# Performance work log

Measured on AMD Instinct MI355X. Metric: run time of the kernel, lower is better.

Reference implementation:

```python
import jax, jax.numpy as jnp
import numpy as np

DIM, D_STATE, D_CONV, EXPAND = 768, 16, 4, 2
D_INNER = EXPAND * DIM
DT_RANK = (DIM + 15) // 16  # 48
B_SZ, L_SZ = 4, 4096


def setup_inputs() -> dict:
    key = jax.random.key(0)
    ks = jax.random.split(key, 20)
    s = 0.02
    d = {}
    d['x'] = jax.random.normal(ks[0], (B_SZ, L_SZ, DIM), jnp.float32)
    d['in_proj_w'] = jax.random.normal(ks[1], (2 * D_INNER, DIM), jnp.float32) * s
    d['out_proj_w'] = jax.random.normal(ks[2], (DIM, D_INNER), jnp.float32) * s
    # forward-direction params
    d['conv1d_w'] = jax.random.normal(ks[3], (D_INNER, 1, D_CONV), jnp.float32) * s
    d['conv1d_bias'] = jax.random.normal(ks[4], (D_INNER,), jnp.float32) * s
    d['x_proj_w'] = jax.random.normal(ks[5], (DT_RANK + 2 * D_STATE, D_INNER), jnp.float32) * s
    d['dt_proj_w'] = jax.random.normal(ks[6], (D_INNER, DT_RANK), jnp.float32) * s
    d['dt_proj_bias'] = jax.random.normal(ks[7], (D_INNER,), jnp.float32) * 0.1 - 4.0
    d['A_log'] = jnp.log(jax.random.uniform(ks[8], (D_INNER, D_STATE), jnp.float32, 1.0, 16.0))
    d['D'] = jax.random.normal(ks[9], (D_INNER,), jnp.float32) * 0.1 + 1.0
    # backward-direction params (bimamba v2)
    d['conv1d_w_b'] = jax.random.normal(ks[10], (D_INNER, 1, D_CONV), jnp.float32) * s
    d['conv1d_bias_b'] = jax.random.normal(ks[11], (D_INNER,), jnp.float32) * s
    d['x_proj_w_b'] = jax.random.normal(ks[12], (DT_RANK + 2 * D_STATE, D_INNER), jnp.float32) * s
    d['dt_proj_w_b'] = jax.random.normal(ks[13], (D_INNER, DT_RANK), jnp.float32) * s
    d['dt_proj_bias_b'] = jax.random.normal(ks[14], (D_INNER,), jnp.float32) * 0.1 - 4.0
    d['A_log_b'] = jnp.log(jax.random.uniform(ks[15], (D_INNER, D_STATE), jnp.float32, 1.0, 16.0))
    d['D_b'] = jax.random.normal(ks[16], (D_INNER,), jnp.float32) * 0.1 + 1.0
    return d


def _causal_depthwise_conv(x, w, b):
    # x: (B, D, L), w: (D, 1, K) depthwise, causal left padding
    k = w.shape[-1]
    xp = jnp.pad(x, ((0, 0), (0, 0), (k - 1, 0)))
    y = jax.lax.conv_general_dilated(
        xp, w, window_strides=(1,), padding='VALID',
        dimension_numbers=('NCH', 'OIH', 'NCH'), feature_group_count=x.shape[1])
    return y + b[None, :, None]


def _selective_scan(u, dt, A, B, C, D):
    # u, dt: (b, d, l); A: (d, n); B, C: (b, n, l); D: (d,)
    b, d, l = u.shape
    n = A.shape[1]

    def step(h, inp):
        u_t, dt_t, B_t, C_t = inp  # (b,d) (b,d) (b,n) (b,n)
        dA = jnp.exp(dt_t[..., None] * A)  # (b,d,n)
        h = h * dA + dt_t[..., None] * B_t[:, None, :] * u_t[..., None]
        y = jnp.einsum('bdn,bn->bd', h, C_t)
        return h, y

    h0 = jnp.zeros((b, d, n), u.dtype)
    xs = (jnp.moveaxis(u, 2, 0), jnp.moveaxis(dt, 2, 0),
          jnp.moveaxis(B, 2, 0), jnp.moveaxis(C, 2, 0))
    _, ys = jax.lax.scan(step, h0, xs)  # ys: (l, b, d)
    y = jnp.moveaxis(ys, 0, 2)  # (b, d, l)
    return y + u * D[None, :, None]


def _one_direction(xz, conv_w, conv_b, x_proj_w, dt_w, dt_b, A_log, D):
    d_inner = xz.shape[1] // 2
    xin, z = xz[:, :d_inner], xz[:, d_inner:]  # (b,d,l) each
    xc = jax.nn.silu(_causal_depthwise_conv(xin, conv_w, conv_b))
    x_dbl = jnp.einsum('bdl,cd->bcl', xc, x_proj_w)  # (b, dt_rank+2n, l)
    dt_r = x_dbl[:, :DT_RANK]
    Bm = x_dbl[:, DT_RANK:DT_RANK + D_STATE]
    Cm = x_dbl[:, DT_RANK + D_STATE:]
    dt = jax.nn.softplus(jnp.einsum('brl,dr->bdl', dt_r, dt_w) + dt_b[None, :, None])
    A = -jnp.exp(A_log)
    y = _selective_scan(xc, dt, A, Bm, Cm, D)
    return y * jax.nn.silu(z)


def reference(x, in_proj_w, out_proj_w,
              conv1d_w, conv1d_bias, x_proj_w, dt_proj_w, dt_proj_bias, A_log, D,
              conv1d_w_b, conv1d_bias_b, x_proj_w_b, dt_proj_w_b, dt_proj_bias_b, A_log_b, D_b):
    # x: (B, L, dim)
    xz = jnp.einsum('bld,ed->bel', x, in_proj_w)  # (b, 2*d_inner, l)
    out_f = _one_direction(xz, conv1d_w, conv1d_bias, x_proj_w,
                           dt_proj_w, dt_proj_bias, A_log, D)
    out_r = _one_direction(xz[:, :, ::-1], conv1d_w_b, conv1d_bias_b, x_proj_w_b,
                           dt_proj_w_b, dt_proj_bias_b, A_log_b, D_b)
    out = out_f + out_r[:, :, ::-1]  # (b, d_inner, l)
    return jnp.einsum('bdl,od->blo', out, out_proj_w)  # (b, l, dim)
```

## Files before the change

### kernel.cpp

```cpp
#include <hip/hip_runtime.h>

#define L_SZ   4096
#define B_SZ   4
#define NCOLS  16384
#define DIM    768
#define DINNER 1536
#define E2     3072
#define DTRANK 48
#define DSTATE 16
#define NCHUNK 64
#define CLEN   64


typedef unsigned short ushortT;
typedef __attribute__((ext_vector_type(8))) short short8;
typedef __attribute__((ext_vector_type(4))) float floatx4;

__device__ __forceinline__ unsigned short f2bf(float f) {
  union { float f; unsigned u; } v; v.f = f;
  unsigned r = v.u + 0x7FFF + ((v.u >> 16) & 1);
  return (unsigned short)(r >> 16);
}
__device__ __forceinline__ float bf2f(unsigned short h) {
  union { unsigned u; float f; } v; v.u = ((unsigned)h) << 16;
  return v.f;
}

__global__ __launch_bounds__(256) void cvt_bf16_kernel(const float* __restrict__ in,
                                                       ushortT* __restrict__ out, int n4) {
  int i = blockIdx.x * 256 + threadIdx.x;
  if (i >= n4) return;
  float4 v = ((const float4*)in)[i];
  ushort4 o;
  o.x = f2bf(v.x); o.y = f2bf(v.y); o.z = f2bf(v.z); o.w = f2bf(v.w);
  ((ushort4*)out)[i] = o;
}

__global__ __launch_bounds__(256) void zero_kernel(float4* __restrict__ p) {
  p[blockIdx.x * 256 + threadIdx.x] = make_float4(0.f, 0.f, 0.f, 0.f);
}

__global__ __launch_bounds__(256) void gemm_nt(const ushortT* __restrict__ A,
                                               const ushortT* __restrict__ Bm,
                                               float* __restrict__ Cf, ushortT* __restrict__ Cb,
                                               int M, int N, int K, int out_bf16, int G)
{
  __shared__ ushortT As[128 * 64];
  __shared__ ushortT Bs[128 * 64];
  int tid = threadIdx.x;
  int wave = tid >> 6, lane = tid & 63;
  int gid = blockIdx.y * gridDim.x + blockIdx.x;
  int per_sg = G * gridDim.y;
  int sg = gid / per_sg, r = gid % per_sg;
  int bm = r / G;
  int bn = sg * G + (r % G);
  const ushortT* Abase = A + (size_t)bm * 128 * K;
  const ushortT* Bbase = Bm + (size_t)bn * 128 * K;
  int lm = lane & 15, lq = lane >> 4;
  int wm = (wave >> 1) * 64, wn = (wave & 1) * 64;
  int rloc = lane >> 3;
  int c_st = (lane & 7) * 8;
  floatx4 acc[4][4] = {};

  for (int k0 = 0; k0 < K; k0 += 64) {
    __syncthreads();
    #pragma unroll
    for (int j = 0; j < 4; j++) {
      int t = wave * 4 + j;
      const ushortT* ga = Abase + (size_t)(t * 8 + rloc) * K + k0 + c_st;
      const ushortT* gb = Bbase + (size_t)(t * 8 + rloc) * K + k0 + c_st;
      __builtin_amdgcn_global_load_lds((const __attribute__((address_space(1))) void*)ga,
                                       (__attribute__((address_space(3))) void*)(As + t * 512),
                                       16, 0, 0);
      __builtin_amdgcn_global_load_lds((const __attribute__((address_space(1))) void*)gb,
                                       (__attribute__((address_space(3))) void*)(Bs + t * 512),
                                       16, 0, 0);
    }
    __syncthreads();
    #pragma unroll
    for (int ks = 0; ks < 2; ks++) {
      short8 af[4], bfv[4];
      #pragma unroll
      for (int i = 0; i < 4; i++)
        af[i] = *(const short8*)(As + (wm + i * 16 + lm) * 64 + ks * 32 + lq * 8);
      #pragma unroll
      for (int j2 = 0; j2 < 4; j2++)
        bfv[j2] = *(const short8*)(Bs + (wn + j2 * 16 + lm) * 64 + ks * 32 + lq * 8);
      #pragma unroll
      for (int i = 0; i < 4; i++)
        #pragma unroll
        for (int j2 = 0; j2 < 4; j2++)
          acc[i][j2] = __builtin_amdgcn_mfma_f32_16x16x32_bf16(af[i], bfv[j2], acc[i][j2], 0, 0, 0);
    }
  }
  #pragma unroll
  for (int i = 0; i < 4; i++) {
    #pragma unroll
    for (int j2 = 0; j2 < 4; j2++) {
      int mg = bm * 128 + wm + i * 16 + lq * 4;
      int ng = bn * 128 + wn + j2 * 16 + lm;
      #pragma unroll
      for (int q = 0; q < 4; q++) {
        size_t off = (size_t)(mg + q) * N + ng;
        if (out_bf16) Cb[off] = f2bf(acc[i][j2][q]);
        else          Cf[off] = acc[i][j2][q];
      }
    }
  }
}

__global__ __launch_bounds__(256) void conv_silu_kernel(const ushortT* __restrict__ xz,
                                                        const float* __restrict__ w,
                                                        const float* __restrict__ bias,
                                                        ushortT* __restrict__ xc, int reverse)
{
  int idx = blockIdx.x * 256 + threadIdx.x;
  int p4 = idx & 1023;
  int rb = idx >> 10;
  int b = rb & 3, d = rb >> 2;
  int wq = p4 >> 6, c = p4 & 63;
  int l0 = c * 64 + wq * 4;
  const ushortT* xin = xz + (size_t)d * NCOLS + b * L_SZ;
  float w0 = w[d * 4], w1 = w[d * 4 + 1], w2 = w[d * 4 + 2], w3 = w[d * 4 + 3];
  float bv = bias[d];
  float xv[8];
  float r0, r1, r2, r3;
  if (!reverse) {
    if (l0 >= 4) {
      ushort4 a = *(const ushort4*)(xin + l0 - 4);
      ushort4 cc = *(const ushort4*)(xin + l0);
      xv[0]=bf2f(a.x); xv[1]=bf2f(a.y); xv[2]=bf2f(a.z); xv[3]=bf2f(a.w);
      xv[4]=bf2f(cc.x); xv[5]=bf2f(cc.y); xv[6]=bf2f(cc.z); xv[7]=bf2f(cc.w);
    } else {
      #pragma unroll
      for (int i = 0; i < 8; i++) { int p = l0 - 4 + i; xv[i] = (p >= 0) ? bf2f(xin[p]) : 0.f; }
    }
    r0 = bv + w0*xv[1] + w1*xv[2] + w2*xv[3] + w3*xv[4];
    r1 = bv + w0*xv[2] + w1*xv[3] + w2*xv[4] + w3*xv[5];
    r2 = bv + w0*xv[3] + w1*xv[4] + w2*xv[5] + w3*xv[6];
    r3 = bv + w0*xv[4] + w1*xv[5] + w2*xv[6] + w3*xv[7];
  } else {
    int base = 4092 - l0;
    if (l0 >= 4) {
      ushort4 a = *(const ushort4*)(xin + base);
      ushort4 cc = *(const ushort4*)(xin + base + 4);
      xv[0]=bf2f(a.x); xv[1]=bf2f(a.y); xv[2]=bf2f(a.z); xv[3]=bf2f(a.w);
      xv[4]=bf2f(cc.x); xv[5]=bf2f(cc.y); xv[6]=bf2f(cc.z); xv[7]=bf2f(cc.w);
    } else {
      #pragma unroll
      for (int i = 0; i < 8; i++) { int p = base + i; xv[i] = (p <= 4095) ? bf2f(xin[p]) : 0.f; }
    }
    r0 = bv + w0*xv[6] + w1*xv[5] + w2*xv[4] + w3*xv[3];
    r1 = bv + w0*xv[5] + w1*xv[4] + w2*xv[3] + w3*xv[2];
    r2 = bv + w0*xv[4] + w1*xv[3] + w2*xv[2] + w3*xv[1];
    r3 = bv + w0*xv[3] + w1*xv[2] + w2*xv[1] + w3*xv[0];
  }
  ushort4 o;
  o.x = f2bf(r0 / (1.f + __expf(-r0)));
  o.y = f2bf(r1 / (1.f + __expf(-r1)));
  o.z = f2bf(r2 / (1.f + __expf(-r2)));
  o.w = f2bf(r3 / (1.f + __expf(-r3)));
  *(ushort4*)(xc + (size_t)d * NCOLS + b * L_SZ + p4 * 4) = o;
}

__global__ __launch_bounds__(256) void xdbl_kernel(const ushortT* __restrict__ xc,
                                                   const float* __restrict__ W,
                                                   float* __restrict__ dtr,
                                                   float* __restrict__ Bt,
                                                   float* __restrict__ Ct)
{
  __shared__ float xcs[32 * 68];
  __shared__ float Ws[80 * 32];
  int tid = threadIdx.x;
  int n0 = blockIdx.x * 64;
  int kbase = blockIdx.y * 512;
  int tm = tid >> 4, tn = tid & 15;
  float acc[5][4] = {};
  for (int k0 = kbase; k0 < kbase + 512; k0 += 32) {
    __syncthreads();
    {
      int kk = tid >> 3, c8 = (tid & 7) * 8;
      const ushortT* src = xc + (size_t)(k0 + kk) * NCOLS + n0 + c8;
      ushort4 a = *(const ushort4*)src;
      ushort4 b = *(const ushort4*)(src + 4);
      float* dst = xcs + kk * 68 + c8;
      dst[0]=bf2f(a.x); dst[1]=bf2f(a.y); dst[2]=bf2f(a.z); dst[3]=bf2f(a.w);
      dst[4]=bf2f(b.x); dst[5]=bf2f(b.y); dst[6]=bf2f(b.z); dst[7]=bf2f(b.w);
    }
    for (int i = tid; i < 80 * 32; i += 256) {
      int m = i >> 5, kk = i & 31;
      Ws[i] = W[(size_t)m * DINNER + k0 + kk];
    }
    __syncthreads();
    #pragma unroll 8
    for (int kk = 0; kk < 32; kk++) {
      const float* xr = xcs + kk * 68 + tn * 4;
      float x0 = xr[0], x1 = xr[1], x2 = xr[2], x3 = xr[3];
      #pragma unroll
      for (int im = 0; im < 5; im++) {
        float wv = Ws[(tm * 5 + im) * 32 + kk];
        acc[im][0] += wv * x0; acc[im][1] += wv * x1;
        acc[im][2] += wv * x2; acc[im][3] += wv * x3;
      }
    }
  }
  #pragma unroll
  for (int im = 0; im < 5; im++) {
    int m = tm * 5 + im;
    #pragma unroll
    for (int j = 0; j < 4; j++) {
      int n = n0 + tn * 4 + j;
      float v = acc[im][j];
      if (m < 48)      atomicAdd(&dtr[(size_t)m * NCOLS + n], v);
      else if (m < 64) atomicAdd(&Bt[(size_t)n * 16 + (m - 48)], v);
      else             atomicAdd(&Ct[(size_t)n * 16 + (m - 64)], v);
    }
  }
}

__global__ __launch_bounds__(256) void dt_kernel(const float* __restrict__ dtr,
                                                 const float* __restrict__ W,
                                                 const float* __restrict__ bias,
                                                 ushortT* __restrict__ dtb)
{
  __shared__ float sD[48 * 68];
  __shared__ float sW[48 * 68];
  int tid = threadIdx.x;
  int n0 = blockIdx.x * 64, d0 = blockIdx.y * 64;
  for (int i = tid; i < 48 * 64; i += 256) {
    int r = i >> 6, c = i & 63;
    sD[r * 68 + c] = dtr[(size_t)r * NCOLS + n0 + c];
  }
  for (int i = tid; i < 64 * 48; i += 256) {
    int dd = i / 48, k = i - dd * 48;
    sW[k * 68 + dd] = W[(size_t)d0 * 48 + i];
  }
  __syncthreads();
  int tn = tid & 15, tm = tid >> 4;
  float acc[4][4];
  #pragma unroll
  for (int i = 0; i < 4; i++) {
    float bv = bias[d0 + tm * 4 + i];
    #pragma unroll
    for (int j = 0; j < 4; j++) acc[i][j] = bv;
  }
  #pragma unroll 6
  for (int k = 0; k < 48; k++) {
    float4 wv = *(const float4*)(sW + k * 68 + tm * 4);
    float4 xv = *(const float4*)(sD + k * 68 + tn * 4);
    float wa[4] = { wv.x, wv.y, wv.z, wv.w };
    float xa[4] = { xv.x, xv.y, xv.z, xv.w };
    #pragma unroll
    for (int i = 0; i < 4; i++)
      #pragma unroll
      for (int j = 0; j < 4; j++)
        acc[i][j] += wa[i] * xa[j];
  }
  #pragma unroll
  for (int i = 0; i < 4; i++) {
    int d = d0 + tm * 4 + i;
    ushort4 o;
    float a0 = acc[i][0], a1 = acc[i][1], a2 = acc[i][2], a3 = acc[i][3];
    o.x = f2bf((a0 > 20.f) ? a0 : log1pf(__expf(a0)));
    o.y = f2bf((a1 > 20.f) ? a1 : log1pf(__expf(a1)));
    o.z = f2bf((a2 > 20.f) ? a2 : log1pf(__expf(a2)));
    o.w = f2bf((a3 > 20.f) ? a3 : log1pf(__expf(a3)));
    *(ushort4*)(dtb + (size_t)d * NCOLS + n0 + tn * 4) = o;
  }
}

__global__ __launch_bounds__(256) void scan_kernel4(ushortT* __restrict__ u,
                                                    const ushortT* __restrict__ dt,
                                                    const float* __restrict__ Bt,
                                                    const float* __restrict__ Ct,
                                                    const float* __restrict__ A_log,
                                                    const float* __restrict__ Dp,
                                                    ushortT* __restrict__ y, int reverse)
{
  __shared__ float Hs[32 * 65];
  __shared__ float Ss[2 * 64];
  int tid = threadIdx.x;
  int hf = tid & 1;
  int c  = (tid >> 1) & 63;
  int dl = tid >> 7;
  int b = blockIdx.y;
  int d = blockIdx.x * 2 + dl;
  int ns0 = hf * 8;

  float Av2[8];
  #pragma unroll
  for (int n = 0; n < 8; n++)
    Av2[n] = -__expf(A_log[d * 16 + ns0 + n]) * 1.442695040888963f;
  float Dv = Dp[d];

  ushortT* ur = u + (size_t)d * NCOLS + b * L_SZ + c * 4;
  const ushortT* tr = dt + (size_t)d * NCOLS + b * L_SZ + c * 4;
  const float*   Bp = Bt + (size_t)b * L_SZ * 16 + ns0;
  const float*   Cp = Ct + (size_t)b * L_SZ * 16 + ns0;

  float h[8];
  float S = 0.f;
  #pragma unroll
  for (int n = 0; n < 8; n++) h[n] = 0.f;

  for (int w = 0; w < 16; w++) {
    ushort4 u4 = *(const ushort4*)(ur + w * 256);
    ushort4 t4 = *(const ushort4*)(tr + w * 256);
    float uv[4] = { bf2f(u4.x), bf2f(u4.y), bf2f(u4.z), bf2f(u4.w) };
    float tv[4] = { bf2f(t4.x), bf2f(t4.y), bf2f(t4.z), bf2f(t4.w) };
    float yo[4];
    #pragma unroll
    for (int q = 0; q < 4; q++) {
      float dtu = tv[q] * uv[q];
      int pl = w * 256 + c * 4 + q;
      const float4* bp4 = (const float4*)(Bp + pl * 16);
      const float4* cp4 = (const float4*)(Cp + pl * 16);
      float4 b0 = bp4[0], b1 = bp4[1];
      float4 c0 = cp4[0], c1 = cp4[1];
      float Bf[8] = { b0.x,b0.y,b0.z,b0.w, b1.x,b1.y,b1.z,b1.w };
      float Cv[8] = { c0.x,c0.y,c0.z,c0.w, c1.x,c1.y,c1.z,c1.w };
      float acc = 0.f;
      #pragma unroll
      for (int n = 0; n < 8; n++) {
        float e = exp2f(tv[q] * Av2[n]);
        h[n] = h[n] * e + Bf[n] * dtu;
        acc += h[n] * Cv[n];
      }
      acc += __shfl_xor(acc, 1);
      yo[q] = acc + Dv * uv[q];
      S += tv[q];
    }
    if (hf == 0) {
      ushort4 o;
      o.x = f2bf(yo[0]); o.y = f2bf(yo[1]); o.z = f2bf(yo[2]); o.w = f2bf(yo[3]);
      *(ushort4*)(ur + w * 256) = o;
    }
  }
  #pragma unroll
  for (int n = 0; n < 8; n++)
    Hs[(dl * 16 + ns0 + n) * 65 + c] = h[n];
  if (hf == 0) Ss[dl * 64 + c] = S;
  __syncthreads();

  if (tid < 32) {
    int dl2 = tid >> 4, n2 = tid & 15;
    float Ac = -__expf(A_log[(blockIdx.x * 2 + dl2) * 16 + n2]) * 1.442695040888963f;
    float hsv = 0.f;
    int row = tid;
    for (int cc = 0; cc < NCHUNK; cc++) {
      int idx = row * 65 + cc;
      float tmp = Hs[idx];
      Hs[idx] = hsv;
      hsv = exp2f(Ac * Ss[dl2 * 64 + cc]) * hsv + tmp;
    }
  }
  __syncthreads();
  float hsr[8];
  #pragma unroll
  for (int n = 0; n < 8; n++) hsr[n] = Hs[(dl * 16 + ns0 + n) * 65 + c];

  ushortT* yrow = y + (size_t)d * NCOLS + b * L_SZ;
  float T = 0.f;
  for (int w = 0; w < 16; w++) {
    ushort4 t4  = *(const ushort4*)(tr + w * 256);
    ushort4 y14 = *(const ushort4*)(ur + w * 256);
    float tv[4]  = { bf2f(t4.x), bf2f(t4.y), bf2f(t4.z), bf2f(t4.w) };
    float y1v[4] = { bf2f(y14.x), bf2f(y14.y), bf2f(y14.z), bf2f(y14.w) };
    float yo[4];
    #pragma unroll
    for (int q = 0; q < 4; q++) {
      T += tv[q];
      int pl = w * 256 + c * 4 + q;
      const float4* cp4 = (const float4*)(Cp + pl * 16);
      float4 c0 = cp4[0], c1 = cp4[1];
      float Cv[8] = { c0.x,c0.y,c0.z,c0.w, c1.x,c1.y,c1.z,c1.w };
      float corr = 0.f;
      #pragma unroll
      for (int n = 0; n < 8; n++)
        corr += (exp2f(Av2[n] * T) * hsr[n]) * Cv[n];
      corr += __shfl_xor(corr, 1);
      yo[q] = y1v[q] + corr;
    }
    if (hf == 0) {
      if (!reverse) {
        ushort4 o;
        o.x = f2bf(yo[0]); o.y = f2bf(yo[1]); o.z = f2bf(yo[2]); o.w = f2bf(yo[3]);
        *(ushort4*)(yrow + w * 256 + c * 4) = o;
      } else {
        ushort4* dst = (ushort4*)(yrow + (15 - w) * 256 + (63 - c) * 4);
        ushort4 old = *dst;
        ushort4 o;
        o.x = f2bf(bf2f(old.x) + yo[3]);
        o.y = f2bf(bf2f(old.y) + yo[2]);
        o.z = f2bf(bf2f(old.z) + yo[1]);
        o.w = f2bf(bf2f(old.w) + yo[0]);
        *dst = o;
      }
    }
  }
}

__global__ __launch_bounds__(256) void inner_kernel(const ushortT* __restrict__ y,
                                                    const ushortT* __restrict__ xz,
                                                    ushortT* __restrict__ innerb)
{
  __shared__ float tile[64 * 65];
  int n0 = blockIdx.x * 64, d0 = blockIdx.y * 64;
  int tid = threadIdx.x;
  int c = tid & 63, rq = tid >> 6;
  int bseg = n0 & ~4095;
  int cch = (n0 & 4095) >> 6;
  int poff = bseg + cch * 4 + (c >> 2) * 256 + (c & 3);
  #pragma unroll
  for (int r = 0; r < 16; r++) {
    int dd = rq + r * 4;
    float yv = bf2f(y[(size_t)(d0 + dd) * NCOLS + poff]);
    float zv = bf2f(xz[(size_t)(DINNER + d0 + dd) * NCOLS + n0 + c]);
    float sv = zv / (1.f + __expf(-zv));
    tile[dd * 65 + c] = yv * sv;
  }
  __syncthreads();
  #pragma unroll
  for (int r = 0; r < 16; r++) {
    int nn = rq + r * 4;
    innerb[(size_t)(n0 + nn) * DINNER + d0 + c] = f2bf(tile[c * 65 + nn]);
  }
}

extern "C" void kernel_launch(void* const* d_in, const int* in_sizes, int n_in,
                              void* d_out, int out_size, void* d_ws, size_t ws_size,
                              hipStream_t stream)
{
  const float* x          = (const float*)d_in[0];
  const float* in_proj_w  = (const float*)d_in[1];
  const float* out_proj_w = (const float*)d_in[2];
  const float* conv_w     = (const float*)d_in[3];
  const float* conv_b     = (const float*)d_in[4];
  const float* xproj_w    = (const float*)d_in[5];
  const float* dt_w       = (const float*)d_in[6];
  const float* dt_b       = (const float*)d_in[7];
  const float* A_log      = (const float*)d_in[8];
  const float* Dp         = (const float*)d_in[9];
  const float* conv_w_b   = (const float*)d_in[10];
  const float* conv_b_b   = (const float*)d_in[11];
  const float* xproj_w_b  = (const float*)d_in[12];
  const float* dt_w_b     = (const float*)d_in[13];
  const float* dt_b_b     = (const float*)d_in[14];
  const float* A_log_b    = (const float*)d_in[15];
  const float* D_b        = (const float*)d_in[16];

  char* ws = (char*)d_ws;
  ushortT* XZ   = (ushortT*)(ws + 0);
  ushortT* XC   = (ushortT*)(ws + 100663296);
  ushortT* YB   = (ushortT*)(ws + 150994944);
  float*   DTR  = (float*)  (ws + 201326592);
  float*   BT   = (float*)  (ws + 204472320);
  float*   CT   = (float*)  (ws + 205520896);
  ushortT* WOB  = (ushortT*)(ws + 206569472);
  ushortT* XB   = (ushortT*)(ws + 100663296);
  ushortT* WIB  = (ushortT*)(ws + 150994944);
  ushortT* DTB  = (ushortT*)d_out;
  ushortT* INNER = XZ;
  float* OUT = (float*)d_out;

  cvt_bf16_kernel<<<12288, 256, 0, stream>>>(x, XB, 3145728);
  cvt_bf16_kernel<<<2304, 256, 0, stream>>>(in_proj_w, WIB, 589824);
  cvt_bf16_kernel<<<1152, 256, 0, stream>>>(out_proj_w, WOB, 294912);

  gemm_nt<<<dim3(128, 24), 256, 0, stream>>>(WIB, XB, nullptr, XZ, E2, NCOLS, DIM, 1, 16);

  conv_silu_kernel<<<24576, 256, 0, stream>>>(XZ, conv_w, conv_b, XC, 0);
  zero_kernel<<<1280, 256, 0, stream>>>((float4*)DTR);
  xdbl_kernel<<<dim3(256, 3), 256, 0, stream>>>(XC, xproj_w, DTR, BT, CT);
  dt_kernel<<<dim3(256, 24), 256, 0, stream>>>(DTR, dt_w, dt_b, DTB);
  scan_kernel4<<<dim3(768, 4), 256, 0, stream>>>(XC, DTB, BT, CT, A_log, Dp, YB, 0);

  conv_silu_kernel<<<24576, 256, 0, stream>>>(XZ, conv_w_b, conv_b_b, XC, 1);
  zero_kernel<<<1280, 256, 0, stream>>>((float4*)DTR);
  xdbl_kernel<<<dim3(256, 3), 256, 0, stream>>>(XC, xproj_w_b, DTR, BT, CT);
  dt_kernel<<<dim3(256, 24), 256, 0, stream>>>(DTR, dt_w_b, dt_b_b, DTB);
  scan_kernel4<<<dim3(768, 4), 256, 0, stream>>>(XC, DTB, BT, CT, A_log_b, D_b, YB, 1);

  inner_kernel<<<dim3(256, 24), 256, 0, stream>>>(YB, XZ, INNER);

  gemm_nt<<<dim3(6, 128), 256, 0, stream>>>(INNER, WOB, OUT, nullptr, NCOLS, DIM, DINNER, 0, 6);
}
```

Measured before the change: 1.761 ms.

## Give each scan thread all 16 states, four channels per block

The selective-scan kernel now assigns all 16 state dimensions to one thread instead of splitting them across a thread pair. This removes the cross-lane shuffle reduction and the half-idle stores, and lets each block cover 4 channels with half as many blocks. The inner dot product is split into four independent accumulators to shorten dependency chains. In exchange, register pressure per thread roughly doubles and there are half as many threads in total, which may reduce occupancy and latency hiding.

```diff
diff --git a/kernel.cpp b/kernel.cpp
--- a/kernel.cpp
+++ b/kernel.cpp
@@ -269,7 +269,7 @@
   }
 }
 
-__global__ __launch_bounds__(256) void scan_kernel4(ushortT* __restrict__ u,
+__global__ __launch_bounds__(256) void scan_kernel5(ushortT* __restrict__ u,
                                                     const ushortT* __restrict__ dt,
                                                     const float* __restrict__ Bt,
                                                     const float* __restrict__ Ct,
@@ -277,87 +277,92 @@
                                                     const float* __restrict__ Dp,
                                                     ushortT* __restrict__ y, int reverse)
 {
-  __shared__ float Hs[32 * 65];
-  __shared__ float Ss[2 * 64];
+  __shared__ float Hs[64 * 65];
+  __shared__ float Ss[4 * 64];
   int tid = threadIdx.x;
-  int hf = tid & 1;
-  int c  = (tid >> 1) & 63;
-  int dl = tid >> 7;
+  int c  = tid & 63;
+  int dl = tid >> 6;
   int b = blockIdx.y;
-  int d = blockIdx.x * 2 + dl;
-  int ns0 = hf * 8;
-
-  float Av2[8];
-  #pragma unroll
-  for (int n = 0; n < 8; n++)
-    Av2[n] = -__expf(A_log[d * 16 + ns0 + n]) * 1.442695040888963f;
+  int d = blockIdx.x * 4 + dl;
+
+  float Av2[16];
+  #pragma unroll
+  for (int n = 0; n < 16; n++)
+    Av2[n] = -__expf(A_log[d * 16 + n]) * 1.442695040888963f;
   float Dv = Dp[d];
 
   ushortT* ur = u + (size_t)d * NCOLS + b * L_SZ + c * 4;
   const ushortT* tr = dt + (size_t)d * NCOLS + b * L_SZ + c * 4;
-  const float*   Bp = Bt + (size_t)b * L_SZ * 16 + ns0;
-  const float*   Cp = Ct + (size_t)b * L_SZ * 16 + ns0;
-
-  float h[8];
+  const float*   Bp = Bt + (size_t)b * L_SZ * 16;
+  const float*   Cp = Ct + (size_t)b * L_SZ * 16;
+
+  float h[16];
+  #pragma unroll
+  for (int n = 0; n < 16; n++) h[n] = 0.f;
   float S = 0.f;
-  #pragma unroll
-  for (int n = 0; n < 8; n++) h[n] = 0.f;
 
   for (int w = 0; w < 16; w++) {
     ushort4 u4 = *(const ushort4*)(ur + w * 256);
     ushort4 t4 = *(const ushort4*)(tr + w * 256);
     float uv[4] = { bf2f(u4.x), bf2f(u4.y), bf2f(u4.z), bf2f(u4.w) };
     float tv[4] = { bf2f(t4.x), bf2f(t4.y), bf2f(t4.z), bf2f(t4.w) };
+    const float4* bp4 = (const float4*)(Bp + (size_t)(w * 256 + c * 4) * 16);
+    const float4* cp4 = (const float4*)(Cp + (size_t)(w * 256 + c * 4) * 16);
     float yo[4];
     #pragma unroll
     for (int q = 0; q < 4; q++) {
-      float dtu = tv[q] * uv[q];
-      int pl = w * 256 + c * 4 + q;
-      const float4* bp4 = (const float4*)(Bp + pl * 16);
-      const float4* cp4 = (const float4*)(Cp + pl * 16);
-      float4 b0 = bp4[0], b1 = bp4[1];
-      float4 c0 = cp4[0], c1 = cp4[1];
-      float Bf[8] = { b0.x,b0.y,b0.z,b0.w, b1.x,b1.y,b1.z,b1.w };
-      float Cv[8] = { c0.x,c0.y,c0.z,c0.w, c1.x,c1.y,c1.z,c1.w };
-      float acc = 0.f;
-      #pragma unroll
-      for (int n = 0; n < 8; n++) {
-        float e = exp2f(tv[q] * Av2[n]);
-        h[n] = h[n] * e + Bf[n] * dtu;
-        acc += h[n] * Cv[n];
+      float tq = tv[q];
+      float dtu = tq * uv[q];
+      float4 b0 = bp4[q * 4 + 0], b1 = bp4[q * 4 + 1], b2 = bp4[q * 4 + 2], b3 = bp4[q * 4 + 3];
+      float4 c0 = cp4[q * 4 + 0], c1 = cp4[q * 4 + 1], c2 = cp4[q * 4 + 2], c3 = cp4[q * 4 + 3];
+      float Bf[16] = { b0.x,b0.y,b0.z,b0.w, b1.x,b1.y,b1.z,b1.w,
+                       b2.x,b2.y,b2.z,b2.w, b3.x,b3.y,b3.z,b3.w };
+      float Cv[16] = { c0.x,c0.y,c0.z,c0.w, c1.x,c1.y,c1.z,c1.w,
+                       c2.x,c2.y,c2.z,c2.w, c3.x,c3.y,c3.z,c3.w };
+      float a0 = 0.f, a1 = 0.f, a2 = 0.f, a3 = 0.f;
+      #pragma unroll
+      for (int n = 0; n < 16; n += 4) {
+        float e0 = exp2f(tq * Av2[n + 0]);
+        float e1 = exp2f(tq * Av2[n + 1]);
+        float e2 = exp2f(tq * Av2[n + 2]);
+        float e3 = exp2f(tq * Av2[n + 3]);
+        h[n + 0] = h[n + 0] * e0 + Bf[n + 0] * dtu;
+        h[n + 1] = h[n + 1] * e1 + Bf[n + 1] * dtu;
+        h[n + 2] = h[n + 2] * e2 + Bf[n + 2] * dtu;
+        h[n + 3] = h[n + 3] * e3 + Bf[n + 3] * dtu;
+        a0 += h[n + 0] * Cv[n + 0];
+        a1 += h[n + 1] * Cv[n + 1];
+        a2 += h[n + 2] * Cv[n + 2];
+        a3 += h[n + 3] * Cv[n + 3];
       }
-      acc += __shfl_xor(acc, 1);
-      yo[q] = acc + Dv * uv[q];
-      S += tv[q];
-    }
-    if (hf == 0) {
-      ushort4 o;
-      o.x = f2bf(yo[0]); o.y = f2bf(yo[1]); o.z = f2bf(yo[2]); o.w = f2bf(yo[3]);
-      *(ushort4*)(ur + w * 256) = o;
-    }
-  }
-  #pragma unroll
-  for (int n = 0; n < 8; n++)
-    Hs[(dl * 16 + ns0 + n) * 65 + c] = h[n];
-  if (hf == 0) Ss[dl * 64 + c] = S;
+      yo[q] = (a0 + a1) + (a2 + a3) + Dv * uv[q];
+      S += tq;
+    }
+    ushort4 o;
+    o.x = f2bf(yo[0]); o.y = f2bf(yo[1]); o.z = f2bf(yo[2]); o.w = f2bf(yo[3]);
+    *(ushort4*)(ur + w * 256) = o;
+  }
+  #pragma unroll
+  for (int n = 0; n < 16; n++)
+    Hs[(dl * 16 + n) * 65 + c] = h[n];
+  Ss[dl * 64 + c] = S;
   __syncthreads();
 
-  if (tid < 32) {
+  if (tid < 64) {
     int dl2 = tid >> 4, n2 = tid & 15;
-    float Ac = -__expf(A_log[(blockIdx.x * 2 + dl2) * 16 + n2]) * 1.442695040888963f;
+    float Ac = -__expf(A_log[(blockIdx.x * 4 + dl2) * 16 + n2]) * 1.442695040888963f;
     float hsv = 0.f;
-    int row = tid;
     for (int cc = 0; cc < NCHUNK; cc++) {
-      int idx = row * 65 + cc;
+      int idx = tid * 65 + cc;
       float tmp = Hs[idx];
       Hs[idx] = hsv;
       hsv = exp2f(Ac * Ss[dl2 * 64 + cc]) * hsv + tmp;
     }
   }
   __syncthreads();
-  float hsr[8];
-  #pragma unroll
-  for (int n = 0; n < 8; n++) hsr[n] = Hs[(dl * 16 + ns0 + n) * 65 + c];
+  float hsr[16];
+  #pragma unroll
+  for (int n = 0; n < 16; n++) hsr[n] = Hs[(dl * 16 + n) * 65 + c];
 
   ushortT* yrow = y + (size_t)d * NCOLS + b * L_SZ;
   float T = 0.f;
@@ -366,36 +371,37 @@
     ushort4 y14 = *(const ushort4*)(ur + w * 256);
     float tv[4]  = { bf2f(t4.x), bf2f(t4.y), bf2f(t4.z), bf2f(t4.w) };
     float y1v[4] = { bf2f(y14.x), bf2f(y14.y), bf2f(y14.z), bf2f(y14.w) };
+    const float4* cp4 = (const float4*)(Cp + (size_t)(w * 256 + c * 4) * 16);
     float yo[4];
     #pragma unroll
     for (int q = 0; q < 4; q++) {
       T += tv[q];
-      int pl = w * 256 + c * 4 + q;
-      const float4* cp4 = (const float4*)(Cp + pl * 16);
-      float4 c0 = cp4[0], c1 = cp4[1];
-      float Cv[8] = { c0.x,c0.y,c0.z,c0.w, c1.x,c1.y,c1.z,c1.w };
-      float corr = 0.f;
-      #pragma unroll
-      for (int n = 0; n < 8; n++)
-        corr += (exp2f(Av2[n] * T) * hsr[n]) * Cv[n];
-      corr += __shfl_xor(corr, 1);
-      yo[q] = y1v[q] + corr;
-    }
-    if (hf == 0) {
-      if (!reverse) {
-        ushort4 o;
-        o.x = f2bf(yo[0]); o.y = f2bf(yo[1]); o.z = f2bf(yo[2]); o.w = f2bf(yo[3]);
-        *(ushort4*)(yrow + w * 256 + c * 4) = o;
-      } else {
-        ushort4* dst = (ushort4*)(yrow + (15 - w) * 256 + (63 - c) * 4);
-        ushort4 old = *dst;
-        ushort4 o;
-        o.x = f2bf(bf2f(old.x) + yo[3]);
-        o.y = f2bf(bf2f(old.y) + yo[2]);
-        o.z = f2bf(bf2f(old.z) + yo[1]);
-        o.w = f2bf(bf2f(old.w) + yo[0]);
-        *dst = o;
+      float4 c0 = cp4[q * 4 + 0], c1 = cp4[q * 4 + 1], c2 = cp4[q * 4 + 2], c3 = cp4[q * 4 + 3];
+      float Cv[16] = { c0.x,c0.y,c0.z,c0.w, c1.x,c1.y,c1.z,c1.w,
+                       c2.x,c2.y,c2.z,c2.w, c3.x,c3.y,c3.z,c3.w };
+      float a0 = 0.f, a1 = 0.f, a2 = 0.f, a3 = 0.f;
+      #pragma unroll
+      for (int n = 0; n < 16; n += 4) {
+        a0 += (exp2f(Av2[n + 0] * T) * hsr[n + 0]) * Cv[n + 0];
+        a1 += (exp2f(Av2[n + 1] * T) * hsr[n + 1]) * Cv[n + 1];
+        a2 += (exp2f(Av2[n + 2] * T) * hsr[n + 2]) * Cv[n + 2];
+        a3 += (exp2f(Av2[n + 3] * T) * hsr[n + 3]) * Cv[n + 3];
       }
+      yo[q] = y1v[q] + (a0 + a1) + (a2 + a3);
+    }
+    if (!reverse) {
+      ushort4 o;
+      o.x = f2bf(yo[0]); o.y = f2bf(yo[1]); o.z = f2bf(yo[2]); o.w = f2bf(yo[3]);
+      *(ushort4*)(yrow + w * 256 + c * 4) = o;
+    } else {
+      ushort4* dst = (ushort4*)(yrow + (15 - w) * 256 + (63 - c) * 4);
+      ushort4 old = *dst;
+      ushort4 o;
+      o.x = f2bf(bf2f(old.x) + yo[3]);
+      o.y = f2bf(bf2f(old.y) + yo[2]);
+      o.z = f2bf(bf2f(old.z) + yo[1]);
+      o.w = f2bf(bf2f(old.w) + yo[0]);
+      *dst = o;
     }
   }
 }
@@ -473,13 +479,13 @@
   zero_kernel<<<1280, 256, 0, stream>>>((float4*)DTR);
   xdbl_kernel<<<dim3(256, 3), 256, 0, stream>>>(XC, xproj_w, DTR, BT, CT);
   dt_kernel<<<dim3(256, 24), 256, 0, stream>>>(DTR, dt_w, dt_b, DTB);
-  scan_kernel4<<<dim3(768, 4), 256, 0, stream>>>(XC, DTB, BT, CT, A_log, Dp, YB, 0);
+  scan_kernel5<<<dim3(384, 4), 256, 0, stream>>>(XC, DTB, BT, CT, A_log, Dp, YB, 0);
 
   conv_silu_kernel<<<24576, 256, 0, stream>>>(XZ, conv_w_b, conv_b_b, XC, 1);
   zero_kernel<<<1280, 256, 0, stream>>>((float4*)DTR);
   xdbl_kernel<<<dim3(256, 3), 256, 0, stream>>>(XC, xproj_w_b, DTR, BT, CT);
   dt_kernel<<<dim3(256, 24), 256, 0, stream>>>(DTR, dt_w_b, dt_b_b, DTB);
-  scan_kernel4<<<dim3(768, 4), 256, 0, stream>>>(XC, DTB, BT, CT, A_log_b, D_b, YB, 1);
+  scan_kernel5<<<dim3(384, 4), 256, 0, stream>>>(XC, DTB, BT, CT, A_log_b, D_b, YB, 1);
 
   inner_kernel<<<dim3(256, 24), 256, 0, stream>>>(YB, XZ, INNER);
 
```

After: 2.145 ms. 21.8% more time.
